# Kernel optimization log

Hardware: AMD Instinct MI355X
Metric: run time of the kernel (lower is better)

Reference implementation:

```python
import jax, jax.numpy as jnp
import numpy as np

K = 16          # neighbors per node
EPS = 1e-5      # BatchNorm eps
BN_SCALE = 1.0 / np.sqrt(1.0 + EPS)  # eval BN with running mean=0, var=1


def _knn_idx(x, k):
    # x: [B, N, d] -> idx [B, N, k] of k nearest neighbors (self excluded)
    sq = jnp.sum(x * x, axis=-1)                               # [B, N]
    d2 = sq[:, :, None] + sq[:, None, :] - 2.0 * jnp.einsum('bnd,bmd->bnm', x, x)
    n = x.shape[1]
    d2 = jnp.where(jnp.eye(n, dtype=bool)[None], jnp.inf, d2)  # no self loops
    _, idx = jax.lax.top_k(-d2, k)
    return idx


def _edge_conv(x, idx, W, b, g, be):
    # PyG EdgeConv: max_j MLP([x_i, x_j - x_i]); MLP = Linear+BN(eval)+ReLU
    xj = jax.vmap(lambda xb, ib: xb[ib])(x, idx)               # [B, N, k, d]
    xi = x[:, :, None, :]
    m = jnp.concatenate([jnp.broadcast_to(xi, xj.shape), xj - xi], axis=-1)
    h = m @ W + b                                              # [B, N, k, out]
    h = g * (h * BN_SCALE) + be                                # eval BatchNorm
    h = jax.nn.relu(h)
    return jnp.max(h, axis=2)                                  # scatter-max over k


def setup_inputs() -> dict:
    key = jax.random.key(0)
    ks = jax.random.split(key, 16)
    B, N, D, C = 128, 256, 6, 12

    def w(k_, shape, fan_in):
        return (jax.random.normal(k_, shape, jnp.float32) / np.sqrt(fan_in)).astype(jnp.float32)

    inp = {
        'x':   jax.random.normal(ks[0], (B, N, D), jnp.float32),
        'W1':  w(ks[1], (2 * 6, 64), 12),   'b1': jnp.zeros((64,), jnp.float32),
        'g1':  jnp.ones((64,), jnp.float32), 'be1': jnp.zeros((64,), jnp.float32),
        'W2':  w(ks[2], (2 * 64, 128), 128), 'b2': jnp.zeros((128,), jnp.float32),
        'g2':  jnp.ones((128,), jnp.float32), 'be2': jnp.zeros((128,), jnp.float32),
        'W3':  w(ks[3], (2 * 128, 256), 256), 'b3': jnp.zeros((256,), jnp.float32),
        'g3':  jnp.ones((256,), jnp.float32), 'be3': jnp.zeros((256,), jnp.float32),
        'Wf1': w(ks[4], (256, 128), 256),    'bf1': jnp.zeros((128,), jnp.float32),
        'gf':  jnp.ones((128,), jnp.float32), 'bef': jnp.zeros((128,), jnp.float32),
        'Wf2': w(ks[5], (128, C), 128),      'bf2': jnp.zeros((C,), jnp.float32),
    }
    return inp


def reference(x, W1, b1, g1, be1, W2, b2, g2, be2, W3, b3, g3, be3,
              Wf1, bf1, gf, bef, Wf2, bf2):
    h = _edge_conv(x, _knn_idx(x, K), W1, b1, g1, be1)   # [B, N, 64]
    h = _edge_conv(h, _knn_idx(h, K), W2, b2, g2, be2)   # [B, N, 128]
    h = _edge_conv(h, _knn_idx(h, K), W3, b3, g3, be3)   # [B, N, 256]
    p = jnp.max(h, axis=1)                               # global_max_pool [B, 256]
    f = jax.nn.relu(gf * ((p @ Wf1 + bf1) * BN_SCALE) + bef)
    return f @ Wf2 + bf2                                 # [B, num_classes]
```

## Files before the change

kernel.cpp:

```cpp
#include <hip/hip_runtime.h>
#include <cstdint>
#include <cstddef>

#define KNN 16
#define NPTS 256
#define NBATCH 128

static constexpr float BN_SCALE_F = 0.9999950000374997f;

__device__ inline unsigned int f32_ord(float f) {
    unsigned int u = __float_as_uint(f);
    return (u & 0x80000000u) ? ~u : (u | 0x80000000u);
}

__device__ __forceinline__ int wmap(int n) { return n + 4 * (n >> 4); }

template<int D>
__global__ __launch_bounds__(256) void sq_kernel(const float* __restrict__ x,
                                                 float* __restrict__ sq) {
    const int t = blockIdx.x * 256 + threadIdx.x;
    const float* r = x + (size_t)t * D;
    float s = 0.f;
    #pragma unroll
    for (int d = 0; d < D; ++d) s = fmaf(r[d], r[d], s);
    sq[t] = s;
}

template<int D>
__global__ __launch_bounds__(256) void knn_fused_kernel(
        const float* __restrict__ x, const float* __restrict__ sq,
        int* __restrict__ idx) {
    constexpr int KS = (D >= 16) ? 16 : D;
    constexpr int NSTEP = D / KS;
    constexpr int NLOADG = (256 * KS + 255) / 256;
    const int t  = threadIdx.x;
    const int tx = t & 15, ty = t >> 4;
    const int srow = t >> 2, sch = t & 3;
    const int b  = blockIdx.x >> 2;
    const int i0 = (blockIdx.x & 3) * 64;
    const int base = b * NPTS;

    __shared__ float Bs[2][KS][260];
    __shared__ float d2L[64][132];
    __shared__ unsigned char Mi[64][68];

    float4 pb[4];
    float  pbs[NLOADG];
    if constexpr (D % 16 == 0) {
        #pragma unroll
        for (int u = 0; u < 4; ++u) {
            const int e = t + u * 256, r = e >> 2, cq = (e & 3) * 4;
            pb[u] = *(const float4*)(x + (size_t)(base + r) * D + cq);
        }
    } else {
        #pragma unroll
        for (int u = 0; u < NLOADG; ++u) {
            const int e = t + u * 256;
            if (e < 256 * KS) {
                const int r = e / KS, c = e % KS;
                pbs[u] = x[(size_t)(base + r) * D + c];
            }
        }
    }

    float sqi[4];
    #pragma unroll
    for (int m = 0; m < 4; ++m) sqi[m] = sq[base + i0 + ty * 4 + m];

    float acc[4][16] = {};

    for (int s = 0; s < NSTEP; ++s) {
        const int buf = s & 1;
        if constexpr (D % 16 == 0) {
            #pragma unroll
            for (int u = 0; u < 4; ++u) {
                const int e = t + u * 256, r = e >> 2, cq = (e & 3) * 4;
                Bs[buf][cq + 0][r] = pb[u].x; Bs[buf][cq + 1][r] = pb[u].y;
                Bs[buf][cq + 2][r] = pb[u].z; Bs[buf][cq + 3][r] = pb[u].w;
            }
        } else {
            #pragma unroll
            for (int u = 0; u < NLOADG; ++u) {
                const int e = t + u * 256;
                if (e < 256 * KS) {
                    const int r = e / KS, c = e % KS;
                    Bs[buf][c][r] = pbs[u];
                }
            }
        }

        if (s + 1 < NSTEP) {
            const int k0n = (s + 1) * KS;
            if constexpr (D % 16 == 0) {
                #pragma unroll
                for (int u = 0; u < 4; ++u) {
                    const int e = t + u * 256, r = e >> 2, cq = (e & 3) * 4;
                    pb[u] = *(const float4*)(x + (size_t)(base + r) * D + k0n + cq);
                }
            } else {
                #pragma unroll
                for (int u = 0; u < NLOADG; ++u) {
                    const int e = t + u * 256;
                    if (e < 256 * KS) {
                        const int r = e / KS, c = e % KS;
                        pbs[u] = x[(size_t)(base + r) * D + k0n + c];
                    }
                }
            }
        }

        __syncthreads();

        #pragma unroll
        for (int kk = 0; kk < KS; ++kk) {
            float am[4], bm[16];
            *(float4*)&am[0] = *(const float4*)&Bs[buf][kk][i0 + ty * 4];
            #pragma unroll
            for (int q = 0; q < 4; ++q)
                *(float4*)&bm[q * 4] = *(const float4*)&Bs[buf][kk][q * 64 + tx * 4];
            #pragma unroll
            for (int m = 0; m < 4; ++m)
                #pragma unroll
                for (int n = 0; n < 16; ++n)
                    acc[m][n] = fmaf(am[m], bm[n], acc[m][n]);
        }
    }

    unsigned int Lv[16], Li[16];
    #pragma unroll
    for (int q = 0; q < 16; ++q) { Lv[q] = 0xFFFFFFFFu; Li[q] = 0u; }

    #pragma unroll
    for (int ph = 0; ph < 2; ++ph) {
        if (ph == 1) __syncthreads();

        float sqj[8];
        #pragma unroll
        for (int w = 0; w < 4; ++w) {
            sqj[w]     = sq[base + ph * 128 + tx * 4 + w];
            sqj[w + 4] = sq[base + ph * 128 + 64 + tx * 4 + w];
        }
        #pragma unroll
        for (int m = 0; m < 4; ++m) {
            const int gi = i0 + ty * 4 + m;
            float o0[4], o1[4];
            #pragma unroll
            for (int w = 0; w < 4; ++w) {
                float v0 = (sqi[m] + sqj[w])     - 2.f * acc[m][8 * ph + w];
                float v1 = (sqi[m] + sqj[w + 4]) - 2.f * acc[m][8 * ph + 4 + w];
                if (gi == ph * 128 + tx * 4 + w)      v0 = INFINITY;
                if (gi == ph * 128 + 64 + tx * 4 + w) v1 = INFINITY;
                o0[w] = v0; o1[w] = v1;
            }
            *(float4*)&d2L[ty * 4 + m][tx * 4]      = make_float4(o0[0], o0[1], o0[2], o0[3]);
            *(float4*)&d2L[ty * 4 + m][64 + tx * 4] = make_float4(o1[0], o1[1], o1[2], o1[3]);
        }
        __syncthreads();

        #pragma unroll 4
        for (int i = 0; i < 32; ++i) {
            const unsigned int v = f32_ord(d2L[srow][sch + 4 * i]);
            const unsigned int j = (unsigned int)(ph * 128 + sch + 4 * i);
            #pragma unroll
            for (int q = 15; q >= 1; --q) {
                const bool a = v < Lv[q];
                const bool c = v < Lv[q - 1];
                Lv[q] = a ? (c ? Lv[q - 1] : v) : Lv[q];
                Li[q] = a ? (c ? Li[q - 1] : j) : Li[q];
            }
            const bool a0 = v < Lv[0];
            Lv[0] = a0 ? v : Lv[0];
            Li[0] = a0 ? j : Li[0];
        }
    }

    __syncthreads();
    #pragma unroll
    for (int q = 0; q < 16; ++q) {
        d2L[srow][sch * 16 + q] = __uint_as_float(Lv[q]);
        Mi[srow][sch * 16 + q]  = (unsigned char)Li[q];
    }
    __syncthreads();

    if (t < 64) {
        const int row = t;
        int h[4];
        unsigned int cv[4], ci[4];
        #pragma unroll
        for (int c = 0; c < 4; ++c) {
            h[c]  = 0;
            cv[c] = __float_as_uint(d2L[row][c * 16]);
            ci[c] = Mi[row][c * 16];
        }
        int outj[16];
        #pragma unroll
        for (int rd = 0; rd < 16; ++rd) {
            unsigned int bv = cv[0], bi = ci[0];
            int bc = 0;
            #pragma unroll
            for (int c = 1; c < 4; ++c) {
                const bool tk = (cv[c] < bv) | ((cv[c] == bv) & (ci[c] < bi));
                bv = tk ? cv[c] : bv;
                bi = tk ? ci[c] : bi;
                bc = tk ? c     : bc;
            }
            outj[rd] = (int)bi;
            #pragma unroll
            for (int c = 0; c < 4; ++c) {
                if (c == bc) {
                    const int hn = h[c] + 1;
                    h[c] = hn;
                    if (hn < 16) {
                        cv[c] = __float_as_uint(d2L[row][c * 16 + hn]);
                        ci[c] = Mi[row][c * 16 + hn];
                    } else {
                        cv[c] = 0xFFFFFFFFu;
                    }
                }
            }
        }
        int4* op = (int4*)(idx + (size_t)(base + i0 + row) * KNN);
        op[0] = make_int4(outj[0],  outj[1],  outj[2],  outj[3]);
        op[1] = make_int4(outj[4],  outj[5],  outj[6],  outj[7]);
        op[2] = make_int4(outj[8],  outj[9],  outj[10], outj[11]);
        op[3] = make_int4(outj[12], outj[13], outj[14], outj[15]);
    }
}

template<int D, int C>
__global__ __launch_bounds__(256) void mlp_gemm_kernel(
        const float* __restrict__ x, const float* __restrict__ W,
        const float* __restrict__ bias, const float* __restrict__ g,
        const float* __restrict__ be,
        float* __restrict__ A, float* __restrict__ Bv) {
    constexpr int BM = 128;
    constexpr int KT = (D >= 16) ? 16 : D;
    constexpr int NSTEP = D / KT;
    constexpr int NXG = (BM * KT + 255) / 256;
    constexpr int NWG = (KT * 128 + 255) / 256;
    const int t  = threadIdx.x;
    const int tx = t & 15;
    const int ty = t >> 4;
    const int m0 = blockIdx.x * BM;
    const int n0 = blockIdx.y * 128;

    __shared__ float Xs[2][KT][132];
    __shared__ float Ws[2][KT][164];

    float acc[8][8] = {};

    const int xr = t >> 1, xc = (t & 1) * 8;
    const int wk = t >> 4, nq = (t & 15) * 8;
    const int gn = n0 + nq;
    const bool isTop = (gn < C);
    const int wcol = isTop ? gn : (gn - C);
    const int mb = wmap(nq);

    float4 px0, px1;
    float4 wt0, wt1, wb0, wb1;
    float  pxg[NXG], pwg[NWG];

    if constexpr (D % 16 == 0) {
        const float* xp = x + (size_t)(m0 + xr) * D + xc;
        px0 = *(const float4*)(xp);
        px1 = *(const float4*)(xp + 4);
        const float* pT = W + (size_t)wk * C + wcol;
        const float* pB = W + (size_t)(D + wk) * C + wcol;
        wt0 = *(const float4*)(pT); wt1 = *(const float4*)(pT + 4);
        wb0 = *(const float4*)(pB); wb1 = *(const float4*)(pB + 4);
    } else {
        #pragma unroll
        for (int u = 0; u < NXG; ++u) {
            const int e = t + u * 256;
            if (e < BM * KT) {
                const int r = e / KT, c = e % KT;
                pxg[u] = x[(size_t)(m0 + r) * D + c];
            }
        }
        #pragma unroll
        for (int u = 0; u < NWG; ++u) {
            const int e = t + u * 256;
            if (e < KT * 128) {
                const int k = e >> 7, n = e & 127;
                const int g2 = n0 + n;
                pwg[u] = (g2 < C)
                    ? W[(size_t)k * C + g2] - W[(size_t)(D + k) * C + g2]
                    : W[(size_t)(D + k) * C + (g2 - C)];
            }
        }
    }

    for (int s = 0; s < NSTEP; ++s) {
        const int buf = s & 1;
        if constexpr (D % 16 == 0) {
            Xs[buf][xc + 0][xr] = px0.x; Xs[buf][xc + 1][xr] = px0.y;
            Xs[buf][xc + 2][xr] = px0.z; Xs[buf][xc + 3][xr] = px0.w;
            Xs[buf][xc + 4][xr] = px1.x; Xs[buf][xc + 5][xr] = px1.y;
            Xs[buf][xc + 6][xr] = px1.z; Xs[buf][xc + 7][xr] = px1.w;
            float4 v0, v1;
            if (isTop) {
                v0 = make_float4(wt0.x - wb0.x, wt0.y - wb0.y,
                                 wt0.z - wb0.z, wt0.w - wb0.w);
                v1 = make_float4(wt1.x - wb1.x, wt1.y - wb1.y,
                                 wt1.z - wb1.z, wt1.w - wb1.w);
            } else {
                v0 = wb0; v1 = wb1;
            }
            *(float4*)&Ws[buf][wk][mb]     = v0;
            *(float4*)&Ws[buf][wk][mb + 4] = v1;
        } else {
            #pragma unroll
            for (int u = 0; u < NXG; ++u) {
                const int e = t + u * 256;
                if (e < BM * KT) {
                    const int r = e / KT, c = e % KT;
                    Xs[buf][c][r] = pxg[u];
                }
            }
            #pragma unroll
            for (int u = 0; u < NWG; ++u) {
                const int e = t + u * 256;
                if (e < KT * 128) {
                    const int k = e >> 7, n = e & 127;
                    Ws[buf][k][wmap(n)] = pwg[u];
                }
            }
        }

        if (s + 1 < NSTEP) {
            const int k0n = (s + 1) * KT;
            if constexpr (D % 16 == 0) {
                const float* xp = x + (size_t)(m0 + xr) * D + k0n + xc;
                px0 = *(const float4*)(xp);
                px1 = *(const float4*)(xp + 4);
                const float* pT = W + (size_t)(k0n + wk) * C + wcol;
                const float* pB = W + (size_t)(D + k0n + wk) * C + wcol;
                wt0 = *(const float4*)(pT); wt1 = *(const float4*)(pT + 4);
                wb0 = *(const float4*)(pB); wb1 = *(const float4*)(pB + 4);
            } else {
                #pragma unroll
                for (int u = 0; u < NXG; ++u) {
                    const int e = t + u * 256;
                    if (e < BM * KT) {
                        const int r = e / KT, c = e % KT;
                        pxg[u] = x[(size_t)(m0 + r) * D + k0n + c];
                    }
                }
                #pragma unroll
                for (int u = 0; u < NWG; ++u) {
                    const int e = t + u * 256;
                    if (e < KT * 128) {
                        const int k = e >> 7, n = e & 127;
                        const int g2 = n0 + n;
                        pwg[u] = (g2 < C)
                            ? W[(size_t)(k0n + k) * C + g2] - W[(size_t)(D + k0n + k) * C + g2]
                            : W[(size_t)(D + k0n + k) * C + (g2 - C)];
                    }
                }
            }
        }

        __syncthreads();

        const int mc = wmap(tx * 8);
        #pragma unroll
        for (int kk = 0; kk < KT; ++kk) {
            float xm[8], wn[8];
            *(float4*)&xm[0] = *(const float4*)&Xs[buf][kk][ty * 8];
            *(float4*)&xm[4] = *(const float4*)&Xs[buf][kk][ty * 8 + 4];
            *(float4*)&wn[0] = *(const float4*)&Ws[buf][kk][mc];
            *(float4*)&wn[4] = *(const float4*)&Ws[buf][kk][mc + 4];
            #pragma unroll
            for (int m = 0; m < 8; ++m)
                #pragma unroll
                for (int n = 0; n < 8; ++n)
                    acc[m][n] = fmaf(xm[m], wn[n], acc[m][n]);
        }
    }

    if (isTop) {
        float fac[8];
        #pragma unroll
        for (int e = 0; e < 8; ++e) fac[e] = g[gn + e] * BN_SCALE_F;
        #pragma unroll
        for (int m = 0; m < 8; ++m) {
            float o[8];
            #pragma unroll
            for (int e = 0; e < 8; ++e) o[e] = fac[e] * acc[m][e];
            float* dst = A + (size_t)(m0 + ty * 8 + m) * C + gn;
            *(float4*)(dst)     = make_float4(o[0], o[1], o[2], o[3]);
            *(float4*)(dst + 4) = make_float4(o[4], o[5], o[6], o[7]);
        }
    } else {
        const int cb = gn - C;
        float fac[8], bb[8], bee[8];
        #pragma unroll
        for (int e = 0; e < 8; ++e) {
            fac[e] = g[cb + e] * BN_SCALE_F;
            bb[e]  = bias[cb + e];
            bee[e] = be[cb + e];
        }
        #pragma unroll
        for (int m = 0; m < 8; ++m) {
            float o[8];
            #pragma unroll
            for (int e = 0; e < 8; ++e)
                o[e] = fmaf(fac[e], acc[m][e] + bb[e], bee[e]);
            float* dst = Bv + (size_t)(m0 + ty * 8 + m) * C + cb;
            *(float4*)(dst)     = make_float4(o[0], o[1], o[2], o[3]);
            *(float4*)(dst + 4) = make_float4(o[4], o[5], o[6], o[7]);
        }
    }
}

template<int C>
__global__ __launch_bounds__(C) void combine_kernel(
        const float* A, const float* __restrict__ Bv,
        const int* __restrict__ idx, float* out) {
    const int bi = blockIdx.x;
    const int c  = threadIdx.x;
    __shared__ int nbr[KNN];
    if (c < KNN) nbr[c] = idx[(size_t)bi * KNN + c];
    __syncthreads();
    const int b0 = bi & ~255;
    float mx = -INFINITY;
    #pragma unroll
    for (int kk = 0; kk < KNN; ++kk)
        mx = fmaxf(mx, Bv[(size_t)(b0 + nbr[kk]) * C + c]);
    float a = A[(size_t)bi * C + c];
    out[(size_t)bi * C + c] = fmaxf(a + mx, 0.f);
}

__global__ __launch_bounds__(256) void head_kernel(
        const float* __restrict__ h3, const float* __restrict__ Wf1,
        const float* __restrict__ bf1, const float* __restrict__ gf,
        const float* __restrict__ bef, const float* __restrict__ Wf2,
        const float* __restrict__ bf2, float* __restrict__ out) {
    const int b   = blockIdx.x;
    const int tid = threadIdx.x;
    __shared__ float p[256];
    __shared__ float f[128];
    const float* hb = h3 + (size_t)b * NPTS * 256;
    float mx = -INFINITY;
    for (int n = 0; n < NPTS; ++n) mx = fmaxf(mx, hb[(size_t)n * 256 + tid]);
    p[tid] = mx;
    __syncthreads();
    if (tid < 128) {
        float acc = bf1[tid];
        for (int d = 0; d < 256; ++d)
            acc = fmaf(p[d], Wf1[(size_t)d * 128 + tid], acc);
        float v = gf[tid] * (acc * BN_SCALE_F) + bef[tid];
        f[tid] = fmaxf(v, 0.f);
    }
    __syncthreads();
    if (tid < 12) {
        float acc = bf2[tid];
        for (int d = 0; d < 128; ++d)
            acc = fmaf(f[d], Wf2[(size_t)d * 12 + tid], acc);
        out[(size_t)b * 12 + tid] = acc;
    }
}

extern "C" void kernel_launch(void* const* d_in, const int* in_sizes, int n_in,
                              void* d_out, int out_size, void* d_ws, size_t ws_size,
                              hipStream_t stream) {
    const float* x   = (const float*)d_in[0];
    const float* W1  = (const float*)d_in[1];
    const float* b1  = (const float*)d_in[2];
    const float* g1  = (const float*)d_in[3];
    const float* be1 = (const float*)d_in[4];
    const float* W2  = (const float*)d_in[5];
    const float* b2  = (const float*)d_in[6];
    const float* g2  = (const float*)d_in[7];
    const float* be2 = (const float*)d_in[8];
    const float* W3  = (const float*)d_in[9];
    const float* b3  = (const float*)d_in[10];
    const float* g3  = (const float*)d_in[11];
    const float* be3 = (const float*)d_in[12];
    const float* Wf1 = (const float*)d_in[13];
    const float* bf1 = (const float*)d_in[14];
    const float* gf  = (const float*)d_in[15];
    const float* bef = (const float*)d_in[16];
    const float* Wf2 = (const float*)d_in[17];
    const float* bf2 = (const float*)d_in[18];
    float* out = (float*)d_out;

    char* ws = (char*)d_ws;
    const size_t idx_bytes = (size_t)NBATCH * NPTS * KNN * sizeof(int);
    const size_t reg_bytes = (size_t)NBATCH * NPTS * 256 * sizeof(float);
    int*   idx = (int*)ws;
    float* R1  = (float*)(ws + idx_bytes);
    float* R2  = (float*)(ws + idx_bytes + reg_bytes);
    float* R3  = (float*)(ws + idx_bytes + 2 * reg_bytes);
    float* sqb = (float*)(ws + idx_bytes + 3 * reg_bytes);

    const int BN = NBATCH * NPTS;
    const int KNN_GRID = NBATCH * 4;
    const int MB = BN / 128;

    sq_kernel<6><<<BN / 256, 256, 0, stream>>>(x, sqb);
    knn_fused_kernel<6><<<KNN_GRID, 256, 0, stream>>>(x, sqb, idx);
    mlp_gemm_kernel<6, 64><<<dim3(MB, 1), 256, 0, stream>>>(
        x, W1, b1, g1, be1, R1, R2);
    combine_kernel<64><<<BN, 64, 0, stream>>>(R1, R2, idx, R1);

    sq_kernel<64><<<BN / 256, 256, 0, stream>>>(R1, sqb);
    knn_fused_kernel<64><<<KNN_GRID, 256, 0, stream>>>(R1, sqb, idx);
    mlp_gemm_kernel<64, 128><<<dim3(MB, 2), 256, 0, stream>>>(
        R1, W2, b2, g2, be2, R2, R3);
    combine_kernel<128><<<BN, 128, 0, stream>>>(R2, R3, idx, R2);

    sq_kernel<128><<<BN / 256, 256, 0, stream>>>(R2, sqb);
    knn_fused_kernel<128><<<KNN_GRID, 256, 0, stream>>>(R2, sqb, idx);
    mlp_gemm_kernel<128, 256><<<dim3(MB, 4), 256, 0, stream>>>(
        R2, W3, b3, g3, be3, R3, R1);
    combine_kernel<256><<<BN, 256, 0, stream>>>(R3, R1, idx, R3);

    head_kernel<<<NBATCH, 256, 0, stream>>>(R3, Wf1, bf1, gf, bef, Wf2, bf2, out);
}
```

Before: 475.8 us.

## Retile kNN to 128-row 512-thread blocks and vectorize combine gather

The kNN kernel now has each block handle 128 query rows with 512 threads, using a separate A tile and an 8x8 per-thread register tile. This halves the number of blocks per batch, so the shared B tile is reloaded less often. The combine kernel now processes several points per 256-thread block with float4 loads, replacing the one-point-per-block scalar launches. The trade-offs are higher shared memory and register use per block in kNN, which may lower occupancy, and only 256 kNN blocks in total.

Result: faster. 433.0 us (-9.0%).

```diff
diff --git a/kernel.cpp b/kernel.cpp
--- a/kernel.cpp
+++ b/kernel.cpp
@@ -27,35 +27,49 @@
 }
 
 template<int D>
-__global__ __launch_bounds__(256) void knn_fused_kernel(
+__global__ __launch_bounds__(512) void knn_fused_kernel(
         const float* __restrict__ x, const float* __restrict__ sq,
         int* __restrict__ idx) {
     constexpr int KS = (D >= 16) ? 16 : D;
     constexpr int NSTEP = D / KS;
-    constexpr int NLOADG = (256 * KS + 255) / 256;
+    constexpr int NLA = (128 * KS + 511) / 512;
+    constexpr int NLB = (256 * KS + 511) / 512;
     const int t  = threadIdx.x;
-    const int tx = t & 15, ty = t >> 4;
-    const int srow = t >> 2, sch = t & 3;
-    const int b  = blockIdx.x >> 2;
-    const int i0 = (blockIdx.x & 3) * 64;
+    const int tx = t & 31, ty = t >> 5;
+    const int sr = t >> 2, sch = t & 3;
+    const int b  = blockIdx.x >> 1;
+    const int i0 = (blockIdx.x & 1) * 128;
     const int base = b * NPTS;
 
+    __shared__ float As[2][KS][132];
     __shared__ float Bs[2][KS][260];
-    __shared__ float d2L[64][132];
-    __shared__ unsigned char Mi[64][68];
-
-    float4 pb[4];
-    float  pbs[NLOADG];
+    __shared__ float d2L[128][132];
+    __shared__ unsigned char Mi[128][68];
+
+    float4 pa, pb[2];
+    float  pas[NLA], pbs[NLB];
     if constexpr (D % 16 == 0) {
-        #pragma unroll
-        for (int u = 0; u < 4; ++u) {
-            const int e = t + u * 256, r = e >> 2, cq = (e & 3) * 4;
+        {
+            const int r = t >> 2, cq = (t & 3) * 4;
+            pa = *(const float4*)(x + (size_t)(base + i0 + r) * D + cq);
+        }
+        #pragma unroll
+        for (int u = 0; u < 2; ++u) {
+            const int e = t + u * 512, r = e >> 2, cq = (e & 3) * 4;
             pb[u] = *(const float4*)(x + (size_t)(base + r) * D + cq);
         }
     } else {
         #pragma unroll
-        for (int u = 0; u < NLOADG; ++u) {
-            const int e = t + u * 256;
+        for (int u = 0; u < NLA; ++u) {
+            const int e = t + u * 512;
+            if (e < 128 * KS) {
+                const int r = e / KS, c = e % KS;
+                pas[u] = x[(size_t)(base + i0 + r) * D + c];
+            }
+        }
+        #pragma unroll
+        for (int u = 0; u < NLB; ++u) {
+            const int e = t + u * 512;
             if (e < 256 * KS) {
                 const int r = e / KS, c = e % KS;
                 pbs[u] = x[(size_t)(base + r) * D + c];
@@ -63,25 +77,38 @@
         }
     }
 
-    float sqi[4];
+    float sqi[8];
     #pragma unroll
-    for (int m = 0; m < 4; ++m) sqi[m] = sq[base + i0 + ty * 4 + m];
-
-    float acc[4][16] = {};
+    for (int m = 0; m < 8; ++m) sqi[m] = sq[base + i0 + ty * 8 + m];
+
+    float acc[8][8] = {};
 
     for (int s = 0; s < NSTEP; ++s) {
         const int buf = s & 1;
         if constexpr (D % 16 == 0) {
-            #pragma unroll
-            for (int u = 0; u < 4; ++u) {
-                const int e = t + u * 256, r = e >> 2, cq = (e & 3) * 4;
+            {
+                const int r = t >> 2, cq = (t & 3) * 4;
+                As[buf][cq + 0][r] = pa.x; As[buf][cq + 1][r] = pa.y;
+                As[buf][cq + 2][r] = pa.z; As[buf][cq + 3][r] = pa.w;
+            }
+            #pragma unroll
+            for (int u = 0; u < 2; ++u) {
+                const int e = t + u * 512, r = e >> 2, cq = (e & 3) * 4;
                 Bs[buf][cq + 0][r] = pb[u].x; Bs[buf][cq + 1][r] = pb[u].y;
                 Bs[buf][cq + 2][r] = pb[u].z; Bs[buf][cq + 3][r] = pb[u].w;
             }
         } else {
             #pragma unroll
-            for (int u = 0; u < NLOADG; ++u) {
-                const int e = t + u * 256;
+            for (int u = 0; u < NLA; ++u) {
+                const int e = t + u * 512;
+                if (e < 128 * KS) {
+                    const int r = e / KS, c = e % KS;
+                    As[buf][c][r] = pas[u];
+                }
+            }
+            #pragma unroll
+            for (int u = 0; u < NLB; ++u) {
+                const int e = t + u * 512;
                 if (e < 256 * KS) {
                     const int r = e / KS, c = e % KS;
                     Bs[buf][c][r] = pbs[u];
@@ -92,15 +119,27 @@
         if (s + 1 < NSTEP) {
             const int k0n = (s + 1) * KS;
             if constexpr (D % 16 == 0) {
-                #pragma unroll
-                for (int u = 0; u < 4; ++u) {
-                    const int e = t + u * 256, r = e >> 2, cq = (e & 3) * 4;
+                {
+                    const int r = t >> 2, cq = (t & 3) * 4;
+                    pa = *(const float4*)(x + (size_t)(base + i0 + r) * D + k0n + cq);
+                }
+                #pragma unroll
+                for (int u = 0; u < 2; ++u) {
+                    const int e = t + u * 512, r = e >> 2, cq = (e & 3) * 4;
                     pb[u] = *(const float4*)(x + (size_t)(base + r) * D + k0n + cq);
                 }
             } else {
                 #pragma unroll
-                for (int u = 0; u < NLOADG; ++u) {
-                    const int e = t + u * 256;
+                for (int u = 0; u < NLA; ++u) {
+                    const int e = t + u * 512;
+                    if (e < 128 * KS) {
+                        const int r = e / KS, c = e % KS;
+                        pas[u] = x[(size_t)(base + i0 + r) * D + k0n + c];
+                    }
+                }
+                #pragma unroll
+                for (int u = 0; u < NLB; ++u) {
+                    const int e = t + u * 512;
                     if (e < 256 * KS) {
                         const int r = e / KS, c = e % KS;
                         pbs[u] = x[(size_t)(base + r) * D + k0n + c];
@@ -113,15 +152,16 @@
 
         #pragma unroll
         for (int kk = 0; kk < KS; ++kk) {
-            float am[4], bm[16];
-            *(float4*)&am[0] = *(const float4*)&Bs[buf][kk][i0 + ty * 4];
-            #pragma unroll
-            for (int q = 0; q < 4; ++q)
-                *(float4*)&bm[q * 4] = *(const float4*)&Bs[buf][kk][q * 64 + tx * 4];
-            #pragma unroll
-            for (int m = 0; m < 4; ++m)
-                #pragma unroll
-                for (int n = 0; n < 16; ++n)
+            float am[8], bm[8];
+            *(float4*)&am[0] = *(const float4*)&As[buf][kk][ty * 8];
+            *(float4*)&am[4] = *(const float4*)&As[buf][kk][ty * 8 + 4];
+            #pragma unroll
+            for (int n = 0; n < 8; ++n)
+                bm[n] = Bs[buf][kk][n * 32 + tx];
+            #pragma unroll
+            for (int m = 0; m < 8; ++m)
+                #pragma unroll
+                for (int n = 0; n < 8; ++n)
                     acc[m][n] = fmaf(am[m], bm[n], acc[m][n]);
         }
     }
@@ -132,34 +172,25 @@
 
     #pragma unroll
     for (int ph = 0; ph < 2; ++ph) {
-        if (ph == 1) __syncthreads();
-
-        float sqj[8];
-        #pragma unroll
-        for (int w = 0; w < 4; ++w) {
-            sqj[w]     = sq[base + ph * 128 + tx * 4 + w];
-            sqj[w + 4] = sq[base + ph * 128 + 64 + tx * 4 + w];
-        }
-        #pragma unroll
-        for (int m = 0; m < 4; ++m) {
-            const int gi = i0 + ty * 4 + m;
-            float o0[4], o1[4];
-            #pragma unroll
-            for (int w = 0; w < 4; ++w) {
-                float v0 = (sqi[m] + sqj[w])     - 2.f * acc[m][8 * ph + w];
-                float v1 = (sqi[m] + sqj[w + 4]) - 2.f * acc[m][8 * ph + 4 + w];
-                if (gi == ph * 128 + tx * 4 + w)      v0 = INFINITY;
-                if (gi == ph * 128 + 64 + tx * 4 + w) v1 = INFINITY;
-                o0[w] = v0; o1[w] = v1;
-            }
-            *(float4*)&d2L[ty * 4 + m][tx * 4]      = make_float4(o0[0], o0[1], o0[2], o0[3]);
-            *(float4*)&d2L[ty * 4 + m][64 + tx * 4] = make_float4(o1[0], o1[1], o1[2], o1[3]);
+        float sqj[4];
+        #pragma unroll
+        for (int n2 = 0; n2 < 4; ++n2)
+            sqj[n2] = sq[base + ph * 128 + n2 * 32 + tx];
+        #pragma unroll
+        for (int m = 0; m < 8; ++m) {
+            const int gi = i0 + ty * 8 + m;
+            #pragma unroll
+            for (int n2 = 0; n2 < 4; ++n2) {
+                float v = (sqi[m] + sqj[n2]) - 2.f * acc[m][ph * 4 + n2];
+                if (gi == ph * 128 + n2 * 32 + tx) v = INFINITY;
+                d2L[ty * 8 + m][n2 * 32 + tx] = v;
+            }
         }
         __syncthreads();
 
         #pragma unroll 4
         for (int i = 0; i < 32; ++i) {
-            const unsigned int v = f32_ord(d2L[srow][sch + 4 * i]);
+            const unsigned int v = f32_ord(d2L[sr][sch + 4 * i]);
             const unsigned int j = (unsigned int)(ph * 128 + sch + 4 * i);
             #pragma unroll
             for (int q = 15; q >= 1; --q) {
@@ -172,17 +203,17 @@
             Lv[0] = a0 ? v : Lv[0];
             Li[0] = a0 ? j : Li[0];
         }
-    }
-
-    __syncthreads();
+        __syncthreads();
+    }
+
     #pragma unroll
     for (int q = 0; q < 16; ++q) {
-        d2L[srow][sch * 16 + q] = __uint_as_float(Lv[q]);
-        Mi[srow][sch * 16 + q]  = (unsigned char)Li[q];
+        d2L[sr][sch * 16 + q] = __uint_as_float(Lv[q]);
+        Mi[sr][sch * 16 + q]  = (unsigned char)Li[q];
     }
     __syncthreads();
 
-    if (t < 64) {
+    if (t < 128) {
         const int row = t;
         int h[4];
         unsigned int cv[4], ci[4];
@@ -414,21 +445,39 @@
 }
 
 template<int C>
-__global__ __launch_bounds__(C) void combine_kernel(
+__global__ __launch_bounds__(256) void combine_kernel(
         const float* A, const float* __restrict__ Bv,
         const int* __restrict__ idx, float* out) {
-    const int bi = blockIdx.x;
-    const int c  = threadIdx.x;
-    __shared__ int nbr[KNN];
-    if (c < KNN) nbr[c] = idx[(size_t)bi * KNN + c];
+    constexpr int CQ = C / 4;
+    constexpr int G  = 256 / CQ;
+    const int tid = threadIdx.x;
+    const int bi0 = blockIdx.x * G;
+    __shared__ int nbr[G * KNN];
+    if (tid < G * KNN) {
+        const int p = tid >> 4, kk = tid & 15;
+        nbr[p * KNN + kk] = idx[(size_t)(bi0 + p) * KNN + kk];
+    }
     __syncthreads();
-    const int b0 = bi & ~255;
-    float mx = -INFINITY;
+    const int p = tid / CQ;
+    const int q = tid % CQ;
+    const int gi = bi0 + p;
+    const int b0 = gi & ~255;
+    const float4* Bv4 = (const float4*)Bv;
+    float4 mx = make_float4(-INFINITY, -INFINITY, -INFINITY, -INFINITY);
     #pragma unroll
-    for (int kk = 0; kk < KNN; ++kk)
-        mx = fmaxf(mx, Bv[(size_t)(b0 + nbr[kk]) * C + c]);
-    float a = A[(size_t)bi * C + c];
-    out[(size_t)bi * C + c] = fmaxf(a + mx, 0.f);
+    for (int kk = 0; kk < KNN; ++kk) {
+        const int r = b0 + nbr[p * KNN + kk];
+        const float4 v = Bv4[(size_t)r * CQ + q];
+        mx.x = fmaxf(mx.x, v.x); mx.y = fmaxf(mx.y, v.y);
+        mx.z = fmaxf(mx.z, v.z); mx.w = fmaxf(mx.w, v.w);
+    }
+    const float4 a = ((const float4*)A)[(size_t)gi * CQ + q];
+    float4 o;
+    o.x = fmaxf(a.x + mx.x, 0.f);
+    o.y = fmaxf(a.y + mx.y, 0.f);
+    o.z = fmaxf(a.z + mx.z, 0.f);
+    o.w = fmaxf(a.w + mx.w, 0.f);
+    ((float4*)out)[(size_t)gi * CQ + q] = o;
 }
 
 __global__ __launch_bounds__(256) void head_kernel(
@@ -495,26 +544,26 @@
     float* sqb = (float*)(ws + idx_bytes + 3 * reg_bytes);
 
     const int BN = NBATCH * NPTS;
-    const int KNN_GRID = NBATCH * 4;
+    const int KNN_GRID = NBATCH * 2;
     const int MB = BN / 128;
 
     sq_kernel<6><<<BN / 256, 256, 0, stream>>>(x, sqb);
-    knn_fused_kernel<6><<<KNN_GRID, 256, 0, stream>>>(x, sqb, idx);
+    knn_fused_kernel<6><<<KNN_GRID, 512, 0, stream>>>(x, sqb, idx);
     mlp_gemm_kernel<6, 64><<<dim3(MB, 1), 256, 0, stream>>>(
         x, W1, b1, g1, be1, R1, R2);
-    combine_kernel<64><<<BN, 64, 0, stream>>>(R1, R2, idx, R1);
+    combine_kernel<64><<<BN / 16, 256, 0, stream>>>(R1, R2, idx, R1);
 
     sq_kernel<64><<<BN / 256, 256, 0, stream>>>(R1, sqb);
-    knn_fused_kernel<64><<<KNN_GRID, 256, 0, stream>>>(R1, sqb, idx);
+    knn_fused_kernel<64><<<KNN_GRID, 512, 0, stream>>>(R1, sqb, idx);
     mlp_gemm_kernel<64, 128><<<dim3(MB, 2), 256, 0, stream>>>(
         R1, W2, b2, g2, be2, R2, R3);
-    combine_kernel<128><<<BN, 128, 0, stream>>>(R2, R3, idx, R2);
+    combine_kernel<128><<<BN / 8, 256, 0, stream>>>(R2, R3, idx, R2);
 
     sq_kernel<128><<<BN / 256, 256, 0, stream>>>(R2, sqb);
-    knn_fused_kernel<128><<<KNN_GRID, 256, 0, stream>>>(R2, sqb, idx);
+    knn_fused_kernel<128><<<KNN_GRID, 512, 0, stream>>>(R2, sqb, idx);
     mlp_gemm_kernel<128, 256><<<dim3(MB, 4), 256, 0, stream>>>(
         R2, W3, b3, g3, be3, R3, R1);
-    combine_kernel<256><<<BN, 256, 0, stream>>>(R3, R1, idx, R3);
+    combine_kernel<256><<<BN / 4, 256, 0, stream>>>(R3, R1, idx, R3);
 
     head_kernel<<<NBATCH, 256, 0, stream>>>(R3, Wf1, bf1, gf, bef, Wf2, bf2, out);
 }
```
